# Performance work log

Hardware: AMD Instinct MI355X
Metric: run time of the kernel (lower is better)

## Reference

```python
import jax, jax.numpy as jnp
import numpy as np

N_HEAD = 16
N_EMBED = 2048


def setup_inputs() -> dict:
    key = jax.random.key(0)
    k1, k2, k3, k4, k5 = jax.random.split(key, 5)
    B, T, C = 4, 2048, N_EMBED
    scale = 1.0 / np.sqrt(C)
    return {
        "x": jax.random.normal(k1, (B, T, C), dtype=jnp.float32),
        "w_attn": jax.random.normal(k2, (C, 3 * C), dtype=jnp.float32) * scale,
        "b_attn": jnp.zeros((3 * C,), dtype=jnp.float32),
        "w_proj": jax.random.normal(k3, (C, C), dtype=jnp.float32) * scale,
        "b_proj": jnp.zeros((C,), dtype=jnp.float32),
    }


def reference(x, w_attn, b_attn, w_proj, b_proj):
    B, T, C = x.shape
    H = N_HEAD
    hd = C // H
    # fused QKV projection: [B,T,3C]
    qkv = jnp.einsum("btc,cd->btd", x, w_attn) + b_attn
    q, k, v = jnp.split(qkv, 3, axis=-1)
    # [B,H,T,hd]
    q = q.reshape(B, T, H, hd).transpose(0, 2, 1, 3)
    k = k.reshape(B, T, H, hd).transpose(0, 2, 1, 3)
    v = v.reshape(B, T, H, hd).transpose(0, 2, 1, 3)
    # scaled dot-product attention (no mask, no dropout at eval)
    scores = jnp.einsum("bhqd,bhkd->bhqk", q, k) / jnp.sqrt(jnp.asarray(hd, dtype=q.dtype))
    attn = jax.nn.softmax(scores, axis=-1)
    y = jnp.einsum("bhqk,bhkd->bhqd", attn, v)
    y = y.transpose(0, 2, 1, 3).reshape(B, T, C)
    return jnp.einsum("btc,cd->btd", y, w_proj) + b_proj
```

## Files before the change

### kernel.cpp

```cpp
#include <hip/hip_runtime.h>
#include <hip/hip_fp16.h>

typedef _Float16 f16;
typedef _Float16 half8 __attribute__((ext_vector_type(8)));
typedef float f32x4 __attribute__((ext_vector_type(4)));

#define NBAT 4
#define NT   2048
#define NC   2048
#define NHEAD 16
#define HD   128
#define NM   8192
#define N3C  6144
#define QK_LD 4096
#define ATT_SCALE 0.088388347648318447f

static __device__ __forceinline__ void gload16(const void* g, void* l) {
  __builtin_amdgcn_global_load_lds(
      (const __attribute__((address_space(1))) unsigned int*)g,
      (__attribute__((address_space(3))) unsigned int*)l, 16, 0, 0);
}


__global__ __launch_bounds__(256) void cvt_x_f16(const float* __restrict__ in,
                                                 f16* __restrict__ out) {
  size_t i = ((size_t)blockIdx.x * 256 + threadIdx.x) * 8;
  float4 a = *(const float4*)(in + i);
  float4 b = *(const float4*)(in + i + 4);
  half8 o;
  o[0] = (f16)a.x; o[1] = (f16)a.y; o[2] = (f16)a.z; o[3] = (f16)a.w;
  o[4] = (f16)b.x; o[5] = (f16)b.y; o[6] = (f16)b.z; o[7] = (f16)b.w;
  *(half8*)(out + i) = o;
}

__global__ __launch_bounds__(256) void cvt_tr_f16(const float* __restrict__ in,
                                                  f16* __restrict__ out,
                                                  int R, int CC) {
  __shared__ float tile[32][33];
  int cb = blockIdx.x * 32, rb = blockIdx.y * 32;
  int lx = threadIdx.x & 31, ly = threadIdx.x >> 5;
  for (int i = 0; i < 32; i += 8)
    tile[ly + i][lx] = in[(size_t)(rb + ly + i) * CC + cb + lx];
  __syncthreads();
  for (int i = 0; i < 32; i += 8)
    out[(size_t)(cb + ly + i) * R + rb + lx] = (f16)tile[lx][ly + i];
}

template <int OUTMODE>
__global__ __launch_bounds__(512, 2)
void gemm256(const f16* __restrict__ A, const f16* __restrict__ BT,
             const float* __restrict__ bias,
             f16* __restrict__ oqk, f16* __restrict__ ovT,
             float* __restrict__ of32, int N, int K, int nbn) {
  __shared__ f16 sA[2][256 * 64];
  __shared__ f16 sB[2][256 * 64];

  const int tid = threadIdx.x;
  const int wv = tid >> 6, lane = tid & 63;
  const int lr = lane & 15, lg = lane >> 4;
  const int wm = wv >> 2, wn = wv & 3;

  const int q8 = gridDim.x >> 3;
  const int sid = ((int)blockIdx.x & 7) * q8 + ((int)blockIdx.x >> 3);
  const int bm = sid / nbn, bn = sid % nbn;

  const int srow = lane >> 3;
  const int schk = (lane & 7) ^ srow;
  const f16* aS = A + (size_t)(bm * 256 + wv * 8 + srow) * K + schk * 8;
  const f16* bS = BT + (size_t)(bn * 256 + wv * 8 + srow) * K + schk * 8;
  const size_t jstep = (size_t)64 * K;

  const int NKT = K >> 6;
  f32x4 acc[8][4] = {};

#pragma unroll
  for (int j = 0; j < 4; ++j) {
    gload16(aS + j * jstep, (void*)(sA[0] + (j * 512 + wv * 64) * 8));
    gload16(bS + j * jstep, (void*)(sB[0] + (j * 512 + wv * 64) * 8));
  }

  for (int kt = 0; kt < NKT; ++kt) {
    const int c = kt & 1;
    if (kt + 1 < NKT) {
      const f16* aN = aS + (size_t)(kt + 1) * 64;
      const f16* bN = bS + (size_t)(kt + 1) * 64;
#pragma unroll
      for (int j = 0; j < 4; ++j) {
        gload16(aN + j * jstep, (void*)(sA[c ^ 1] + (j * 512 + wv * 64) * 8));
        gload16(bN + j * jstep, (void*)(sB[c ^ 1] + (j * 512 + wv * 64) * 8));
      }
      asm volatile("s_waitcnt vmcnt(8)" ::: "memory");
    } else {
      asm volatile("s_waitcnt vmcnt(0)" ::: "memory");
    }
    __builtin_amdgcn_s_barrier();
    asm volatile("" ::: "memory");

    const f16* pa = sA[c] + (wm * 128 + lr) * 64;
    const f16* pb = sB[c] + (wn * 64 + lr) * 64;
#pragma unroll
    for (int ks = 0; ks < 2; ++ks) {
      const int xc = ((ks * 4 + lg) ^ (lr & 7)) * 8;
      half8 a[8], b[4];
#pragma unroll
      for (int mf = 0; mf < 8; ++mf)
        a[mf] = *(const half8*)(pa + mf * (16 * 64) + xc);
#pragma unroll
      for (int nf = 0; nf < 4; ++nf)
        b[nf] = *(const half8*)(pb + nf * (16 * 64) + xc);
#pragma unroll
      for (int mf = 0; mf < 8; ++mf)
#pragma unroll
        for (int nf = 0; nf < 4; ++nf)
          acc[mf][nf] = __builtin_amdgcn_mfma_f32_16x16x32_f16(
              a[mf], b[nf], acc[mf][nf], 0, 0, 0);
    }
    asm volatile("" ::: "memory");
    __builtin_amdgcn_s_barrier();
  }

#pragma unroll
  for (int nf = 0; nf < 4; ++nf) {
    const int col = bn * 256 + wn * 64 + nf * 16 + lr;
    const float bv = bias[col];
#pragma unroll
    for (int mf = 0; mf < 8; ++mf) {
      const int row0 = bm * 256 + wm * 128 + mf * 16 + lg * 4;
      f32x4 v = acc[mf][nf];
      if (OUTMODE == 0) {
#pragma unroll
        for (int r = 0; r < 4; ++r)
          of32[(size_t)(row0 + r) * N + col] = v[r] + bv;
      } else {
        if (col < 4096) {
#pragma unroll
          for (int r = 0; r < 4; ++r)
            oqk[(size_t)(row0 + r) * QK_LD + col] = (f16)(v[r] + bv);
        } else {
          const int dfull = col - 4096;
          const int hh = dfull >> 7, dd = dfull & 127;
#pragma unroll
          for (int r = 0; r < 4; ++r) {
            const int row = row0 + r;
            const int bb = row >> 11, tt = row & 2047;
            ovT[((size_t)(bb * NHEAD + hh) * HD + dd) * NT + tt] = (f16)(v[r] + bv);
          }
        }
      }
    }
  }
}

__global__ __launch_bounds__(256, 2)
void attn_fwd(const f16* __restrict__ qk, const f16* __restrict__ vT,
              f16* __restrict__ y) {
  const int bid = blockIdx.x;
  const int sid = (bid & 7) * 128 + (bid >> 3);
  const int qt = sid & 15;
  const int bh = sid >> 4;
  const int b = bh >> 4, h = bh & 15;
  const int tid = threadIdx.x, w = tid >> 6, lane = tid & 63;
  const int lr = lane & 15, lg = lane >> 4;

  __shared__ f16 Ks[2][64 * 128];
  __shared__ f16 Vs[2][128 * 64];
  __shared__ f16 Ps[4][2][16 * 64];

  half8 qf[2][4];
  for (int s = 0; s < 2; ++s) {
    const f16* qp = qk + (size_t)(b * NT + qt * 128 + w * 32 + s * 16 + lr) * QK_LD +
                    h * HD + lg * 8;
    for (int dc = 0; dc < 4; ++dc) qf[s][dc] = *(const half8*)(qp + dc * 32);
  }

  f32x4 accy[2][8] = {};
  f32x4 lacc[2] = {};
  float mrow[2][4];
  for (int s = 0; s < 2; ++s)
    for (int r = 0; r < 4; ++r) mrow[s][r] = -1e30f;

  half8 onev;
  for (int j = 0; j < 8; ++j) onev[j] = (f16)1.0f;

  const char* kbase[4];
  const char* vbase[4];
  for (int j = 0; j < 4; ++j) {
    int idx = w * 4 + j;
    {
      int row = idx * 4 + lg;
      int swz = (lr * 16) ^ ((row & 7) << 4);
      kbase[j] = (const char*)qk +
                 ((size_t)(b * NT + row) * QK_LD + 2048 + h * HD) * 2 + swz;
    }
    {
      int d = idx * 8 + (lane >> 3);
      int cj = (lane & 7) ^ (d & 7);
      vbase[j] = (const char*)vT + ((size_t)(bh * HD + d) * NT + cj * 8) * 2;
    }
  }

  for (int j = 0; j < 4; ++j) {
    int idx = w * 4 + j;
    gload16(kbase[j], (void*)((char*)Ks[0] + idx * 1024));
    gload16(vbase[j], (void*)((char*)Vs[0] + idx * 1024));
  }
  __syncthreads();

  int cur = 0;
  for (int kt = 0; kt < 32; ++kt) {
    if (kt + 1 < 32) {
      for (int j = 0; j < 4; ++j) {
        int idx = w * 4 + j;
        gload16(kbase[j] + (size_t)(kt + 1) * (64 * QK_LD * 2),
                (void*)((char*)Ks[cur ^ 1] + idx * 1024));
        gload16(vbase[j] + (size_t)(kt + 1) * 128,
                (void*)((char*)Vs[cur ^ 1] + idx * 1024));
      }
    }

    f32x4 sa[2][4] = {};
    for (int nb = 0; nb < 4; ++nb) {
      int kvr = nb * 16 + lr;
      const char* kr = (const char*)Ks[cur] + kvr * 256;
      int s7 = (kvr & 7) << 4;
      for (int dc = 0; dc < 4; ++dc) {
        half8 kb = *(const half8*)(kr + ((dc * 64 + lg * 16) ^ s7));
        sa[0][nb] = __builtin_amdgcn_mfma_f32_16x16x32_f16(qf[0][dc], kb, sa[0][nb], 0, 0, 0);
        sa[1][nb] = __builtin_amdgcn_mfma_f32_16x16x32_f16(qf[1][dc], kb, sa[1][nb], 0, 0, 0);
      }
    }

    for (int s = 0; s < 2; ++s) {
      float sv[4][4];
      float pml[4] = {-1e30f, -1e30f, -1e30f, -1e30f};
      for (int nb = 0; nb < 4; ++nb)
        for (int r = 0; r < 4; ++r) {
          float x = sa[s][nb][r] * ATT_SCALE;
          sv[nb][r] = x;
          pml[r] = fmaxf(pml[r], x);
        }
      bool ok = true;
      for (int r = 0; r < 4; ++r) ok &= (pml[r] <= mrow[s][r] + 8.0f);
      if (!__all(ok)) {
        for (int r = 0; r < 4; ++r) {
          for (int off = 1; off < 16; off <<= 1)
            pml[r] = fmaxf(pml[r], __shfl_xor(pml[r], off));
          float mn = fmaxf(mrow[s][r], pml[r]);
          float al = __expf(mrow[s][r] - mn);
          mrow[s][r] = mn;
          lacc[s][r] *= al;
          for (int db = 0; db < 8; ++db) accy[s][db][r] *= al;
        }
      }
      for (int nb = 0; nb < 4; ++nb)
        for (int r = 0; r < 4; ++r) {
          float p = __expf(sv[nb][r] - mrow[s][r]);
          int prow = lg * 4 + r;
          int chunk = (nb * 2 + (lr >> 3)) ^ (prow & 7);
          Ps[w][s][prow * 64 + chunk * 8 + (lr & 7)] = (f16)p;
        }
    }

    half8 pa[2][2];
    for (int s = 0; s < 2; ++s)
      for (int kc = 0; kc < 2; ++kc) {
        int chunk = (kc * 4 + lg) ^ (lr & 7);
        pa[s][kc] = *(const half8*)(&Ps[w][s][lr * 64 + chunk * 8]);
      }
    for (int s = 0; s < 2; ++s)
      for (int kc = 0; kc < 2; ++kc)
        lacc[s] = __builtin_amdgcn_mfma_f32_16x16x32_f16(pa[s][kc], onev, lacc[s], 0, 0, 0);

    for (int db = 0; db < 8; ++db) {
      int d = db * 16 + lr;
      const char* vr = (const char*)Vs[cur] + d * 128;
      int d7 = d & 7;
      for (int kc = 0; kc < 2; ++kc) {
        half8 vb = *(const half8*)(vr + (((kc * 4 + lg) ^ d7) * 16));
        accy[0][db] = __builtin_amdgcn_mfma_f32_16x16x32_f16(pa[0][kc], vb, accy[0][db], 0, 0, 0);
        accy[1][db] = __builtin_amdgcn_mfma_f32_16x16x32_f16(pa[1][kc], vb, accy[1][db], 0, 0, 0);
      }
    }

    __syncthreads();
    cur ^= 1;
  }

  for (int s = 0; s < 2; ++s) {
    f32x4 inv;
    for (int r = 0; r < 4; ++r) inv[r] = 1.0f / lacc[s][r];
    f16* yp = y + (size_t)(b * NT + qt * 128 + w * 32 + s * 16 + lg * 4) * NC +
              h * HD + lr;
    for (int db = 0; db < 8; ++db)
      for (int r = 0; r < 4; ++r)
        yp[(size_t)r * NC + db * 16] = (f16)(accy[s][db][r] * inv[r]);
  }
}

extern "C" void kernel_launch(void* const* d_in, const int* in_sizes, int n_in,
                              void* d_out, int out_size, void* d_ws, size_t ws_size,
                              hipStream_t stream) {
  (void)in_sizes; (void)n_in; (void)out_size; (void)ws_size;
  const float* x      = (const float*)d_in[0];
  const float* w_attn = (const float*)d_in[1];
  const float* b_attn = (const float*)d_in[2];
  const float* w_proj = (const float*)d_in[3];
  const float* b_proj = (const float*)d_in[4];
  float* out = (float*)d_out;

  char* p = (char*)d_ws;
  f16* xh  = (f16*)p; p += (size_t)NM * NC * 2;
  f16* waT = (f16*)p; p += (size_t)N3C * NC * 2;
  f16* wpT = (f16*)p; p += (size_t)NC * NC * 2;
  f16* qkb = (f16*)p; p += (size_t)NM * QK_LD * 2;
  f16* vT  = (f16*)p; p += (size_t)NBAT * NHEAD * HD * NT * 2;
  f16* yh  = (f16*)p; p += (size_t)NM * NC * 2;

  cvt_x_f16<<<8192, 256, 0, stream>>>(x, xh);
  cvt_tr_f16<<<dim3(192, 64), 256, 0, stream>>>(w_attn, waT, NC, N3C);
  cvt_tr_f16<<<dim3(64, 64), 256, 0, stream>>>(w_proj, wpT, NC, NC);
  gemm256<1><<<768, 512, 0, stream>>>(xh, waT, b_attn, qkb, vT, nullptr,
                                      N3C, NC, 24);
  attn_fwd<<<1024, 256, 0, stream>>>(qkb, vT, yh);
  gemm256<0><<<256, 512, 0, stream>>>(yh, wpT, b_proj, nullptr, nullptr,
                                      out, NC, NC, 8);
}
```

Before: 496.9 us.

## Restructure GEMM pipeline to load fragments to registers before issuing next-tile prefetch

Reworks the 256x256 GEMM mainloop so each k-tile's A and B fragments are read from LDS into registers up front. A barrier follows, then the next tiles are prefetched into the freed buffers while the MFMAs run. B is staged two tiles ahead and A one tile ahead, with a vmcnt(4) wait. The LDS layout is split into 128-row halves and the per-thread staging mapping is reorganised. Block-to-tile mapping is also changed to group tiles per XCD. Holding all fragments in registers raises register pressure, and the extra barrier per iteration may cost some of the overlap gained.

```diff
diff --git a/kernel.cpp b/kernel.cpp
--- a/kernel.cpp
+++ b/kernel.cpp
@@ -52,71 +52,83 @@
              const float* __restrict__ bias,
              f16* __restrict__ oqk, f16* __restrict__ ovT,
              float* __restrict__ of32, int N, int K, int nbn) {
-  __shared__ f16 sA[2][256 * 64];
-  __shared__ f16 sB[2][256 * 64];
+  __shared__ f16 sA[2][2][128 * 64];
+  __shared__ f16 sB[2][2][128 * 64];
 
   const int tid = threadIdx.x;
   const int wv = tid >> 6, lane = tid & 63;
   const int lr = lane & 15, lg = lane >> 4;
   const int wm = wv >> 2, wn = wv & 3;
 
-  const int q8 = gridDim.x >> 3;
-  const int sid = ((int)blockIdx.x & 7) * q8 + ((int)blockIdx.x >> 3);
-  const int bm = sid / nbn, bn = sid % nbn;
-
-  const int srow = lane >> 3;
-  const int schk = (lane & 7) ^ srow;
-  const f16* aS = A + (size_t)(bm * 256 + wv * 8 + srow) * K + schk * 8;
-  const f16* bS = BT + (size_t)(bn * 256 + wv * 8 + srow) * K + schk * 8;
-  const size_t jstep = (size_t)64 * K;
+  const int bid = blockIdx.x;
+  const int xcd = bid & 7, li = bid >> 3;
+  const int bm = (xcd & 3) * 8 + (li & 7);
+  const int bn = (xcd >> 2) * (nbn >> 1) + (li >> 3);
+
+  const int srow = tid >> 3;
+  const int schk = (tid & 7) ^ (srow & 7);
+  const f16* aBase = A + (size_t)(bm * 256 + srow) * K + schk * 8;
+  const f16* bBase = BT + (size_t)(bn * 256 + srow) * K + schk * 8;
+  const int ldst = tid * 8;
+  const size_t rs64 = (size_t)64 * K, rs128 = (size_t)128 * K;
 
   const int NKT = K >> 6;
   f32x4 acc[8][4] = {};
 
-#pragma unroll
-  for (int j = 0; j < 4; ++j) {
-    gload16(aS + j * jstep, (void*)(sA[0] + (j * 512 + wv * 64) * 8));
-    gload16(bS + j * jstep, (void*)(sB[0] + (j * 512 + wv * 64) * 8));
-  }
+  auto stgA = [&](int t, int buf) {
+#pragma unroll
+    for (int hf = 0; hf < 2; ++hf)
+#pragma unroll
+      for (int j = 0; j < 2; ++j)
+        gload16(aBase + hf * rs128 + j * rs64 + t * 64,
+                (void*)(&sA[buf][hf][j * 4096 + ldst]));
+  };
+  auto stgB = [&](int t, int buf) {
+#pragma unroll
+    for (int hf = 0; hf < 2; ++hf)
+#pragma unroll
+      for (int j = 0; j < 2; ++j)
+        gload16(bBase + hf * rs128 + j * rs64 + t * 64,
+                (void*)(&sB[buf][hf][j * 4096 + ldst]));
+  };
+
+  stgB(0, 0); stgA(0, 0); stgB(1, 1);
 
   for (int kt = 0; kt < NKT; ++kt) {
     const int c = kt & 1;
-    if (kt + 1 < NKT) {
-      const f16* aN = aS + (size_t)(kt + 1) * 64;
-      const f16* bN = bS + (size_t)(kt + 1) * 64;
-#pragma unroll
-      for (int j = 0; j < 4; ++j) {
-        gload16(aN + j * jstep, (void*)(sA[c ^ 1] + (j * 512 + wv * 64) * 8));
-        gload16(bN + j * jstep, (void*)(sB[c ^ 1] + (j * 512 + wv * 64) * 8));
-      }
-      asm volatile("s_waitcnt vmcnt(8)" ::: "memory");
-    } else {
-      asm volatile("s_waitcnt vmcnt(0)" ::: "memory");
-    }
+    if (kt < NKT - 1) asm volatile("s_waitcnt vmcnt(4)" ::: "memory");
+    else              asm volatile("s_waitcnt vmcnt(0)" ::: "memory");
     __builtin_amdgcn_s_barrier();
     asm volatile("" ::: "memory");
 
-    const f16* pa = sA[c] + (wm * 128 + lr) * 64;
-    const f16* pb = sB[c] + (wn * 64 + lr) * 64;
+    const f16* pa = &sA[c][wm][lr * 64];
+    const f16* pb = &sB[c][wn >> 1][((wn & 1) * 64 + lr) * 64];
+    half8 a[8][2], b[4][2];
 #pragma unroll
     for (int ks = 0; ks < 2; ++ks) {
       const int xc = ((ks * 4 + lg) ^ (lr & 7)) * 8;
-      half8 a[8], b[4];
 #pragma unroll
       for (int mf = 0; mf < 8; ++mf)
-        a[mf] = *(const half8*)(pa + mf * (16 * 64) + xc);
+        a[mf][ks] = *(const half8*)(pa + mf * 1024 + xc);
 #pragma unroll
       for (int nf = 0; nf < 4; ++nf)
-        b[nf] = *(const half8*)(pb + nf * (16 * 64) + xc);
-#pragma unroll
-      for (int mf = 0; mf < 8; ++mf)
-#pragma unroll
-        for (int nf = 0; nf < 4; ++nf)
+        b[nf][ks] = *(const half8*)(pb + nf * 1024 + xc);
+    }
+    asm volatile("s_waitcnt lgkmcnt(0)" ::: "memory");
+    __builtin_amdgcn_s_barrier();
+    asm volatile("" ::: "memory");
+
+    if (kt + 1 < NKT) stgA(kt + 1, c ^ 1);
+    if (kt + 2 < NKT) stgB(kt + 2, c);
+
+#pragma unroll
+    for (int mf = 0; mf < 8; ++mf)
+#pragma unroll
+      for (int nf = 0; nf < 4; ++nf)
+#pragma unroll
+        for (int ks = 0; ks < 2; ++ks)
           acc[mf][nf] = __builtin_amdgcn_mfma_f32_16x16x32_f16(
-              a[mf], b[nf], acc[mf][nf], 0, 0, 0);
-    }
-    asm volatile("" ::: "memory");
-    __builtin_amdgcn_s_barrier();
+              a[mf][ks], b[nf][ks], acc[mf][nf], 0, 0, 0);
   }
 
 #pragma unroll
```

New measurement: 507.7 us. 1.02x slower.

## Deepen GEMM pipeline to four 32-wide K stages and fix attention load waits

Applied to the files above, without the earlier changes.

The GEMM now uses a four-slot ring of 32-wide K sub-tiles, with loads issued two sub-stages ahead after compute rather than a simple double buffer. It also changes block-to-tile mapping so each XCD covers a contiguous 8-row band and half the columns, aiming for better L2 locality. In attention, the __syncthreads after the initial prefetch is replaced by explicit vmcnt waits plus raw barriers inside the loop, so the next tile's loads can overlap compute instead of the compiler draining them. The GEMM's shared memory footprint stays the same, and correctness depends on the hand-counted vmcnt values and the new swizzle layout.

```diff
diff --git a/kernel.cpp b/kernel.cpp
--- a/kernel.cpp
+++ b/kernel.cpp
@@ -52,62 +52,63 @@
              const float* __restrict__ bias,
              f16* __restrict__ oqk, f16* __restrict__ ovT,
              float* __restrict__ of32, int N, int K, int nbn) {
-  __shared__ f16 sA[2][256 * 64];
-  __shared__ f16 sB[2][256 * 64];
+  __shared__ f16 sA[4 * 8192];
+  __shared__ f16 sB[4 * 8192];
 
   const int tid = threadIdx.x;
   const int wv = tid >> 6, lane = tid & 63;
   const int lr = lane & 15, lg = lane >> 4;
   const int wm = wv >> 2, wn = wv & 3;
 
-  const int q8 = gridDim.x >> 3;
-  const int sid = ((int)blockIdx.x & 7) * q8 + ((int)blockIdx.x >> 3);
-  const int bm = sid / nbn, bn = sid % nbn;
-
-  const int srow = lane >> 3;
-  const int schk = (lane & 7) ^ srow;
-  const f16* aS = A + (size_t)(bm * 256 + wv * 8 + srow) * K + schk * 8;
-  const f16* bS = BT + (size_t)(bn * 256 + wv * 8 + srow) * K + schk * 8;
-  const size_t jstep = (size_t)64 * K;
-
-  const int NKT = K >> 6;
+  const int bid = blockIdx.x;
+  const int xcd = bid & 7, li = bid >> 3;
+  const int nbh = nbn >> 1;
+  const int bm = (xcd & 3) * 8 + (li & 7);
+  const int bn = (xcd >> 2) * nbh + (li >> 3);
+
+  const int q0 = tid >> 3;
+  const int cx = (tid & 7) ^ (q0 & 7);
+  const int shi = cx >> 2, skc = cx & 3;
+  const f16* aSrc = A + (size_t)(bm * 256 + q0 + 128 * shi) * K + skc * 8;
+  const f16* bSrc = BT + (size_t)(bn * 256 + q0 + 128 * shi) * K + skc * 8;
+  const size_t rs64 = (size_t)64 * K;
+  const int ldsOff = tid * 8;
+
+  const int NSUB = K >> 5, NKT = K >> 6;
   f32x4 acc[8][4] = {};
 
-#pragma unroll
-  for (int j = 0; j < 4; ++j) {
-    gload16(aS + j * jstep, (void*)(sA[0] + (j * 512 + wv * 64) * 8));
-    gload16(bS + j * jstep, (void*)(sB[0] + (j * 512 + wv * 64) * 8));
-  }
+  auto stage = [&](int s) {
+    const int sl = (s & 3) * 8192;
+    const int sk = s * 32;
+#pragma unroll
+    for (int j = 0; j < 2; ++j) {
+      gload16(aSrc + j * rs64 + sk, (void*)(sA + sl + j * 4096 + ldsOff));
+      gload16(bSrc + j * rs64 + sk, (void*)(sB + sl + j * 4096 + ldsOff));
+    }
+  };
+
+  stage(0); stage(1); stage(2); stage(3);
+
+  const int ca = ((wm * 4 + lg) ^ (lr & 7)) * 8;
+  const int cb = (((wn >> 1) * 4 + lg) ^ (lr & 7)) * 8;
 
   for (int kt = 0; kt < NKT; ++kt) {
-    const int c = kt & 1;
-    if (kt + 1 < NKT) {
-      const f16* aN = aS + (size_t)(kt + 1) * 64;
-      const f16* bN = bS + (size_t)(kt + 1) * 64;
-#pragma unroll
-      for (int j = 0; j < 4; ++j) {
-        gload16(aN + j * jstep, (void*)(sA[c ^ 1] + (j * 512 + wv * 64) * 8));
-        gload16(bN + j * jstep, (void*)(sB[c ^ 1] + (j * 512 + wv * 64) * 8));
-      }
-      asm volatile("s_waitcnt vmcnt(8)" ::: "memory");
-    } else {
-      asm volatile("s_waitcnt vmcnt(0)" ::: "memory");
-    }
+    if (kt < NKT - 1) asm volatile("s_waitcnt vmcnt(8)" ::: "memory");
+    else              asm volatile("s_waitcnt vmcnt(0)" ::: "memory");
     __builtin_amdgcn_s_barrier();
     asm volatile("" ::: "memory");
 
-    const f16* pa = sA[c] + (wm * 128 + lr) * 64;
-    const f16* pb = sB[c] + (wn * 64 + lr) * 64;
 #pragma unroll
     for (int ks = 0; ks < 2; ++ks) {
-      const int xc = ((ks * 4 + lg) ^ (lr & 7)) * 8;
+      const f16* pa = sA + ((2 * kt + ks) & 3) * 8192;
+      const f16* pb = sB + ((2 * kt + ks) & 3) * 8192;
       half8 a[8], b[4];
 #pragma unroll
       for (int mf = 0; mf < 8; ++mf)
-        a[mf] = *(const half8*)(pa + mf * (16 * 64) + xc);
+        a[mf] = *(const half8*)(pa + (mf * 16 + lr) * 64 + ca);
 #pragma unroll
       for (int nf = 0; nf < 4; ++nf)
-        b[nf] = *(const half8*)(pb + nf * (16 * 64) + xc);
+        b[nf] = *(const half8*)(pb + ((wn & 1) * 64 + nf * 16 + lr) * 64 + cb);
 #pragma unroll
       for (int mf = 0; mf < 8; ++mf)
 #pragma unroll
@@ -117,6 +118,9 @@
     }
     asm volatile("" ::: "memory");
     __builtin_amdgcn_s_barrier();
+
+    if (2 * kt + 4 < NSUB) stage(2 * kt + 4);
+    if (2 * kt + 5 < NSUB) stage(2 * kt + 5);
   }
 
 #pragma unroll
@@ -204,7 +208,6 @@
     gload16(kbase[j], (void*)((char*)Ks[0] + idx * 1024));
     gload16(vbase[j], (void*)((char*)Vs[0] + idx * 1024));
   }
-  __syncthreads();
 
   int cur = 0;
   for (int kt = 0; kt < 32; ++kt) {
@@ -217,6 +220,10 @@
                 (void*)((char*)Vs[cur ^ 1] + idx * 1024));
       }
     }
+    if (kt < 31) asm volatile("s_waitcnt vmcnt(8)" ::: "memory");
+    else         asm volatile("s_waitcnt vmcnt(0)" ::: "memory");
+    __builtin_amdgcn_s_barrier();
+    asm volatile("" ::: "memory");
 
     f32x4 sa[2][4] = {};
     for (int nb = 0; nb < 4; ++nb) {
@@ -282,7 +289,8 @@
       }
     }
 
-    __syncthreads();
+    asm volatile("" ::: "memory");
+    __builtin_amdgcn_s_barrier();
     cur ^= 1;
   }
 
```

New measurement: 553.1 us. 1.11x slower.
